# Kernel tuning notes

Hardware: AMD Instinct MI355X
Metric: run time of the kernel (lower is better)

## Reference

```python
import math
import jax, jax.numpy as jnp
import numpy as np

IMAGE_SIZE = 224


def _resize_bilinear(img, out_h, out_w):
    """PyTorch F.interpolate(mode='bilinear', align_corners=False) equivalent.
    img: [B, H, W] -> [B, out_h, out_w]. No antialiasing (matches torch default)."""
    B, H, W = img.shape

    def coords(out, size):
        r = jnp.maximum((jnp.arange(out, dtype=jnp.float32) + 0.5) * (size / out) - 0.5, 0.0)
        i0 = jnp.minimum(jnp.floor(r).astype(jnp.int32), size - 1)
        i1 = jnp.minimum(i0 + 1, size - 1)
        w = r - i0.astype(jnp.float32)
        return i0, i1, w

    r0, r1, wr = coords(out_h, H)
    c0, c1, wc = coords(out_w, W)
    rows = img[:, r0, :] * (1.0 - wr)[None, :, None] + img[:, r1, :] * wr[None, :, None]
    out = rows[:, :, c0] * (1.0 - wc)[None, None, :] + rows[:, :, c1] * wc[None, None, :]
    return out


def _normalize_minmax(x, eps=1e-8):
    mn = x.min()
    mx = x.max()
    return jnp.where(mx - mn < eps, jnp.zeros_like(x), (x - mn) / (mx - mn + eps))


def _grid_embed(vals, n):
    """Row-major scatter of vals[:, :n] into a ceil(sqrt(n))^2 grid (zero padded)."""
    B = vals.shape[0]
    gs = int(math.ceil(math.sqrt(n)))
    pad = gs * gs - n
    return jnp.pad(vals, ((0, 0), (0, pad))).reshape(B, gs, gs)


def setup_inputs() -> dict:
    key = jax.random.key(0)
    hidden_state = jax.random.normal(key, (32, 512, 4096, 1), dtype=jnp.float32)
    return {"hidden_state": hidden_state}


def reference(hidden_state):
    B, E, N, _ = hidden_state.shape
    x = hidden_state[..., 0]  # [B, E, N]

    # temporal view: mean over nodes -> [B, E] -> grid -> resize
    t_grid = _grid_embed(x.mean(axis=2), E)
    temporal = _normalize_minmax(_resize_bilinear(t_grid, IMAGE_SIZE, IMAGE_SIZE))

    # spatial view: mean over embedding dim -> [B, N] -> grid -> resize
    s_grid = _grid_embed(x.mean(axis=1), N)
    spatial = _normalize_minmax(_resize_bilinear(s_grid, IMAGE_SIZE, IMAGE_SIZE))

    # correlation view: row-normalized centered features, [B, E, E] correlation
    xc = x - x.mean(axis=2, keepdims=True)
    xn = xc / (jnp.linalg.norm(xc, axis=2, keepdims=True) + 1e-8)
    corr = jnp.einsum('bin,bjn->bij', xn, xn)  # [B, E, E]
    correlation = _normalize_minmax(_resize_bilinear(corr, IMAGE_SIZE, IMAGE_SIZE))

    # [B, 3, image_size, image_size]
    return jnp.stack([temporal, spatial, correlation], axis=1)
```

## Files before the change

kernel.cpp:

```cpp
#include <hip/hip_runtime.h>
#include <hip/hip_bf16.h>
#include <math.h>

#define IMG 224
#define PIX (IMG*IMG)
#define B_ 32
#define E_ 512
#define N_ 4096
#define SV_BLOCKS 256
#define SC_ ((float)(512.0/224.0))
#define RPB 16
#define NCHUNK 32

typedef __attribute__((ext_vector_type(8))) short bf16x8;
typedef __attribute__((ext_vector_type(4))) float f32x4;

__device__ inline unsigned short f2bf(float f){
  unsigned u = __float_as_uint(f);
  unsigned r = (u + 0x7FFFu + ((u >> 16) & 1u)) >> 16;
  return (unsigned short)r;
}

__global__ void __launch_bounds__(256) stats_y(const float* __restrict__ x,
                                               float* __restrict__ meanv,
                                               float* __restrict__ colpart,
                                               ushort* __restrict__ y){
  int b = blockIdx.x >> 5, chunk = blockIdx.x & 31;
  int e0 = chunk << 4;
  int t = threadIdx.x;
  __shared__ short sInv[512];
  __shared__ float sW[224];
  __shared__ float red[2][16];
  sInv[t] = -1; sInv[t + 256] = -1;
  __syncthreads();
  if (t < 224){
    float r = fmaxf(((float)t + 0.5f) * SC_ - 0.5f, 0.f);
    int r0 = min((int)r, E_ - 1);
    sW[t] = r - (float)r0;
    sInv[r0] = (short)t;
  }
  __syncthreads();

  float cur[16], prev[16], nxt[16], csum[16];
  #pragma unroll
  for (int j = 0; j < 16; j++){ csum[j] = 0.f; prev[j] = 0.f; }
  const float4* row0 = (const float4*)(x + ((size_t)b * E_ + e0) * N_);
  #pragma unroll
  for (int k = 0; k < 4; k++) *(float4*)(cur + 4 * k) = row0[t + 256 * k];
  float pmu = 0.f, prn = 0.f;

  for (int idx = 0; idx <= RPB; idx++){
    int e = e0 + idx;
    if (e >= E_) break;
    bool hasNext = (idx < RPB) && (e + 1 < E_);
    if (hasNext){
      const float4* nr = (const float4*)(x + ((size_t)b * E_ + e + 1) * N_);
      #pragma unroll
      for (int k = 0; k < 4; k++) *(float4*)(nxt + 4 * k) = nr[t + 256 * k];
    }
    float s = 0.f, ss = 0.f;
    #pragma unroll
    for (int j = 0; j < 16; j++){ s += cur[j]; ss += cur[j] * cur[j]; }
    #pragma unroll
    for (int o = 32; o; o >>= 1){ s += __shfl_down(s, o); ss += __shfl_down(ss, o); }
    int wv = t >> 6, ln = t & 63, p = idx & 1;
    if (ln == 0){ red[p][wv] = s; red[p][8 + wv] = ss; }
    __syncthreads();
    float S  = red[p][0] + red[p][1] + red[p][2] + red[p][3];
    float SS = red[p][8] + red[p][9] + red[p][10] + red[p][11];
    float mu = S * (1.f / N_);
    float var = fmaxf(SS - S * S * (1.f / N_), 0.f);
    float rn = 1.f / (sqrtf(var) + 1e-8f);
    if (idx < RPB){
      #pragma unroll
      for (int j = 0; j < 16; j++) csum[j] += cur[j];
      if (t == 0) meanv[b * E_ + e] = mu;
    }
    if (idx >= 1){
      int i = sInv[e - 1];
      if (i >= 0){
        float w = sW[i];
        float a0 = (1.f - w) * prn, a1 = w * rn;
        float cc = -(a0 * pmu + a1 * mu);
        ushort* yo = y + ((size_t)b * IMG + i) * N_;
        #pragma unroll
        for (int k = 0; k < 4; k++){
          union { ushort u[4]; int2 v; } pk;
          #pragma unroll
          for (int j = 0; j < 4; j++)
            pk.u[j] = f2bf(a0 * prev[4*k+j] + a1 * cur[4*k+j] + cc);
          *(int2*)(yo + 1024 * k + 4 * t) = pk.v;
        }
      }
    }
    pmu = mu; prn = rn;
    #pragma unroll
    for (int j = 0; j < 16; j++){ prev[j] = cur[j]; if (hasNext) cur[j] = nxt[j]; }
  }
  float* cp = colpart + ((size_t)(b * NCHUNK + chunk)) * N_;
  #pragma unroll
  for (int k = 0; k < 4; k++) *(float4*)(cp + 1024 * k + 4 * t) = *(float4*)(csum + 4 * k);
}

__global__ void __launch_bounds__(256) col_finalize(const float* __restrict__ colpart,
                                                    float* __restrict__ colmean){
  int b = blockIdx.x >> 4;
  int n = ((blockIdx.x & 15) << 8) + threadIdx.x;
  float s = 0.f;
  #pragma unroll
  for (int c = 0; c < NCHUNK; c++) s += colpart[((size_t)(b * NCHUNK + c)) * N_ + n];
  colmean[b * N_ + n] = s * (1.f / E_);
}

__device__ inline float grid_val(const float* v, int gs, int n, int r, int c){
  int idx = r * gs + c;
  return (idx < n) ? v[idx] : 0.f;
}
__device__ inline float bilin(const float* v, int gs, int n, int i, int j){
  float sc = (float)((double)gs / 224.0);
  float r = fmaxf(((float)i + 0.5f) * sc - 0.5f, 0.f);
  float c = fmaxf(((float)j + 0.5f) * sc - 0.5f, 0.f);
  int r0 = min((int)r, gs - 1), c0 = min((int)c, gs - 1);
  int r1 = min(r0 + 1, gs - 1), c1 = min(c0 + 1, gs - 1);
  float wr = r - (float)r0, wc = c - (float)c0;
  float v00 = grid_val(v, gs, n, r0, c0), v10 = grid_val(v, gs, n, r1, c0);
  float v01 = grid_val(v, gs, n, r0, c1), v11 = grid_val(v, gs, n, r1, c1);
  float ra = v00 * (1.f - wr) + v10 * wr;
  float rb = v01 * (1.f - wr) + v11 * wr;
  return ra * (1.f - wc) + rb * wc;
}

__global__ void __launch_bounds__(256) small_views(const float* __restrict__ meanv,
                                                   const float* __restrict__ colmean,
                                                   float* __restrict__ out,
                                                   float* __restrict__ scr){
  float tmn = INFINITY, tmx = -INFINITY, smn = INFINITY, smx = -INFINITY;
  for (int g = blockIdx.x * 256 + threadIdx.x; g < B_ * PIX; g += SV_BLOCKS * 256){
    int b = g / PIX, p = g - b * PIX;
    int i = p / IMG, j = p - i * IMG;
    float tv = bilin(meanv   + b * E_, 23, E_, i, j);
    float sv = bilin(colmean + b * N_, 64, N_, i, j);
    out[((size_t)b * 3 + 0) * PIX + p] = tv;
    out[((size_t)b * 3 + 1) * PIX + p] = sv;
    tmn = fminf(tmn, tv); tmx = fmaxf(tmx, tv);
    smn = fminf(smn, sv); smx = fmaxf(smx, sv);
  }
  #pragma unroll
  for (int o = 32; o; o >>= 1){
    tmn = fminf(tmn, __shfl_down(tmn, o)); tmx = fmaxf(tmx, __shfl_down(tmx, o));
    smn = fminf(smn, __shfl_down(smn, o)); smx = fmaxf(smx, __shfl_down(smx, o));
  }
  __shared__ float red[4][4];
  int wv = threadIdx.x >> 6, ln = threadIdx.x & 63;
  if (ln == 0){ red[wv][0] = tmn; red[wv][1] = tmx; red[wv][2] = smn; red[wv][3] = smx; }
  __syncthreads();
  if (threadIdx.x == 0){
    scr[blockIdx.x * 4 + 0] = fminf(fminf(red[0][0], red[1][0]), fminf(red[2][0], red[3][0]));
    scr[blockIdx.x * 4 + 1] = fmaxf(fmaxf(red[0][1], red[1][1]), fmaxf(red[2][1], red[3][1]));
    scr[blockIdx.x * 4 + 2] = fminf(fminf(red[0][2], red[1][2]), fminf(red[2][2], red[3][2]));
    scr[blockIdx.x * 4 + 3] = fmaxf(fmaxf(red[0][3], red[1][3]), fmaxf(red[2][3], red[3][3]));
  }
}

#define LDSTR 72
__global__ void __launch_bounds__(256) corr_gemm(const ushort* __restrict__ y,
                                                 float* __restrict__ out,
                                                 float* __restrict__ scr){
  const int TI[10] = {0,0,0,0,1,1,1,2,2,3};
  const int TJ[10] = {0,1,2,3,1,2,3,2,3,3};
  int b = blockIdx.x / 10;
  int tile = blockIdx.x - b * 10;
  int ti = TI[tile], tj = TJ[tile];
  bool diag = (ti == tj);
  const ushort* yb = y + (size_t)b * IMG * N_;
  __shared__ ushort lA[64 * LDSTR];
  __shared__ ushort lB[64 * LDSTR];
  int t = threadIdx.x;
  int wv = t >> 6, ln = t & 63;
  int wm = wv & 1, wn = wv >> 1;
  int quad = ln >> 4, l16 = ln & 15;
  f32x4 acc[2][2] = {};
  int s = t & 7, r2 = t >> 3;
  int rA0 = min(ti * 64 + r2,      223), rA1 = min(ti * 64 + r2 + 32, 223);
  int rB0 = min(tj * 64 + r2,      223), rB1 = min(tj * 64 + r2 + 32, 223);
  for (int k0 = 0; k0 < N_; k0 += 64){
    int4 a0 = *(const int4*)(yb + (size_t)rA0 * N_ + k0 + s * 8);
    int4 a1 = *(const int4*)(yb + (size_t)rA1 * N_ + k0 + s * 8);
    int4 b0v = *(const int4*)(yb + (size_t)rB0 * N_ + k0 + s * 8);
    int4 b1v = *(const int4*)(yb + (size_t)rB1 * N_ + k0 + s * 8);
    __syncthreads();
    *(int4*)(lA + r2 * LDSTR + s * 8)        = a0;
    *(int4*)(lA + (r2 + 32) * LDSTR + s * 8) = a1;
    *(int4*)(lB + r2 * LDSTR + s * 8)        = b0v;
    *(int4*)(lB + (r2 + 32) * LDSTR + s * 8) = b1v;
    __syncthreads();
    #pragma unroll
    for (int kk = 0; kk < 2; kk++){
      bf16x8 af0 = *(const bf16x8*)(lA + (wm * 32 + l16)      * LDSTR + kk * 32 + quad * 8);
      bf16x8 af1 = *(const bf16x8*)(lA + (wm * 32 + 16 + l16) * LDSTR + kk * 32 + quad * 8);
      bf16x8 bf0 = *(const bf16x8*)(lB + (wn * 32 + l16)      * LDSTR + kk * 32 + quad * 8);
      bf16x8 bf1 = *(const bf16x8*)(lB + (wn * 32 + 16 + l16) * LDSTR + kk * 32 + quad * 8);
      acc[0][0] = __builtin_amdgcn_mfma_f32_16x16x32_bf16(af0, bf0, acc[0][0], 0, 0, 0);
      acc[0][1] = __builtin_amdgcn_mfma_f32_16x16x32_bf16(af0, bf1, acc[0][1], 0, 0, 0);
      acc[1][0] = __builtin_amdgcn_mfma_f32_16x16x32_bf16(af1, bf0, acc[1][0], 0, 0, 0);
      acc[1][1] = __builtin_amdgcn_mfma_f32_16x16x32_bf16(af1, bf1, acc[1][1], 0, 0, 0);
    }
  }
  float mn = INFINITY, mx = -INFINITY;
  float* ov = out + ((size_t)b * 3 + 2) * PIX;
  #pragma unroll
  for (int im = 0; im < 2; im++)
    #pragma unroll
    for (int in = 0; in < 2; in++){
      int gi0 = ti * 64 + wm * 32 + im * 16 + quad * 4;
      int gj  = tj * 64 + wn * 32 + in * 16 + l16;
      #pragma unroll
      for (int rg = 0; rg < 4; rg++){
        int gi = gi0 + rg;
        if (gi < IMG && gj < IMG){
          float v = acc[im][in][rg];
          ov[gi * IMG + gj] = v;
          mn = fminf(mn, v); mx = fmaxf(mx, v);
        }
      }
      if (!diag && gj < IMG && gi0 < IMG){
        float4 tv;
        tv.x = acc[im][in][0]; tv.y = acc[im][in][1];
        tv.z = acc[im][in][2]; tv.w = acc[im][in][3];
        *(float4*)(ov + gj * IMG + gi0) = tv;
      }
    }
  #pragma unroll
  for (int o = 32; o; o >>= 1){
    mn = fminf(mn, __shfl_down(mn, o)); mx = fmaxf(mx, __shfl_down(mx, o));
  }
  __shared__ float red[4][2];
  if (ln == 0){ red[wv][0] = mn; red[wv][1] = mx; }
  __syncthreads();
  if (t == 0){
    scr[(b * 10 + tile) * 2 + 0] = fminf(fminf(red[0][0], red[1][0]), fminf(red[2][0], red[3][0]));
    scr[(b * 10 + tile) * 2 + 1] = fmaxf(fmaxf(red[0][1], red[1][1]), fmaxf(red[2][1], red[3][1]));
  }
}

__global__ void __launch_bounds__(256) reduce_slots(const float* __restrict__ sv_scr,
                                                    const float* __restrict__ corr_scr,
                                                    float* __restrict__ slots){
  int t = threadIdx.x;
  float tmn = sv_scr[4*t+0], tmx = sv_scr[4*t+1];
  float smn = sv_scr[4*t+2], smx = sv_scr[4*t+3];
  float cmn = INFINITY, cmx = -INFINITY;
  for (int idx = t; idx < B_ * 10; idx += 256){
    cmn = fminf(cmn, corr_scr[2*idx]);
    cmx = fmaxf(cmx, corr_scr[2*idx+1]);
  }
  #pragma unroll
  for (int o = 32; o; o >>= 1){
    tmn = fminf(tmn, __shfl_down(tmn, o)); tmx = fmaxf(tmx, __shfl_down(tmx, o));
    smn = fminf(smn, __shfl_down(smn, o)); smx = fmaxf(smx, __shfl_down(smx, o));
    cmn = fminf(cmn, __shfl_down(cmn, o)); cmx = fmaxf(cmx, __shfl_down(cmx, o));
  }
  __shared__ float red[4][6];
  int wv = t >> 6, ln = t & 63;
  if (ln == 0){
    red[wv][0]=tmn; red[wv][1]=tmx; red[wv][2]=smn;
    red[wv][3]=smx; red[wv][4]=cmn; red[wv][5]=cmx;
  }
  __syncthreads();
  if (t == 0){
    slots[0] = fminf(fminf(red[0][0],red[1][0]), fminf(red[2][0],red[3][0]));
    slots[1] = fmaxf(fmaxf(red[0][1],red[1][1]), fmaxf(red[2][1],red[3][1]));
    slots[2] = fminf(fminf(red[0][2],red[1][2]), fminf(red[2][2],red[3][2]));
    slots[3] = fmaxf(fmaxf(red[0][3],red[1][3]), fmaxf(red[2][3],red[3][3]));
    slots[4] = fminf(fminf(red[0][4],red[1][4]), fminf(red[2][4],red[3][4]));
    slots[5] = fmaxf(fmaxf(red[0][5],red[1][5]), fmaxf(red[2][5],red[3][5]));
  }
}

__global__ void __launch_bounds__(256) normalize_k(float* __restrict__ out,
                                                   const float* __restrict__ slots){
  int g = blockIdx.x * 256 + threadIdx.x;
  if (g >= B_ * 3 * PIX) return;
  int view = (g / PIX) % 3;
  float mn = slots[2 * view];
  float mx = slots[2 * view + 1];
  float d = mx - mn;
  float v = out[g];
  out[g] = (d < 1e-8f) ? 0.f : (v - mn) / (d + 1e-8f);
}

extern "C" void kernel_launch(void* const* d_in, const int* in_sizes, int n_in,
                              void* d_out, int out_size, void* d_ws, size_t ws_size,
                              hipStream_t stream){
  const float* x = (const float*)d_in[0];
  float* out = (float*)d_out;
  char* ws = (char*)d_ws;
  float* slots    = (float*)(ws + 0);
  float* meanv    = (float*)(ws + 256);
  float* colmean  = meanv + B_ * E_;
  float* colpart  = colmean + B_ * N_;
  float* sv_scr   = colpart + (size_t)B_ * NCHUNK * N_;
  float* corr_scr = sv_scr + SV_BLOCKS * 4;
  size_t y_off = ((size_t)((char*)(corr_scr + B_ * 10 * 2) - ws) + 255) & ~(size_t)255;
  ushort* y = (ushort*)(ws + y_off);

  hipLaunchKernelGGL(stats_y, dim3(B_ * NCHUNK), dim3(256), 0, stream,
                     x, meanv, colpart, y);
  hipLaunchKernelGGL(col_finalize, dim3(B_ * 16), dim3(256), 0, stream,
                     colpart, colmean);
  hipLaunchKernelGGL(small_views, dim3(SV_BLOCKS), dim3(256), 0, stream,
                     meanv, colmean, out, sv_scr);
  hipLaunchKernelGGL(corr_gemm, dim3(B_ * 10), dim3(256), 0, stream,
                     y, out, corr_scr);
  hipLaunchKernelGGL(reduce_slots, dim3(1), dim3(256), 0, stream,
                     sv_scr, corr_scr, slots);
  hipLaunchKernelGGL(normalize_k, dim3((B_ * 3 * PIX + 255) / 256), dim3(256), 0, stream,
                     out, slots);
}
```

Before: 464.1 us.

## Split correlation GEMM along K into four partial blocks plus reduce kernel

```diff
diff --git a/kernel.cpp b/kernel.cpp
--- a/kernel.cpp
+++ b/kernel.cpp
@@ -11,6 +11,9 @@
 #define SC_ ((float)(512.0/224.0))
 #define RPB 16
 #define NCHUNK 32
+#define KSPLIT 4
+#define KLEN (N_/KSPLIT)
+#define NTILE 10
 
 typedef __attribute__((ext_vector_type(8))) short bf16x8;
 typedef __attribute__((ext_vector_type(4))) float f32x4;
@@ -163,16 +166,16 @@
 }
 
 #define LDSTR 72
-__global__ void __launch_bounds__(256) corr_gemm(const ushort* __restrict__ y,
-                                                 float* __restrict__ out,
-                                                 float* __restrict__ scr){
-  const int TI[10] = {0,0,0,0,1,1,1,2,2,3};
-  const int TJ[10] = {0,1,2,3,1,2,3,2,3,3};
-  int b = blockIdx.x / 10;
-  int tile = blockIdx.x - b * 10;
-  int ti = TI[tile], tj = TJ[tile];
-  bool diag = (ti == tj);
-  const ushort* yb = y + (size_t)b * IMG * N_;
+__device__ const int TI_[NTILE] = {0,0,0,0,1,1,1,2,2,3};
+__device__ const int TJ_[NTILE] = {0,1,2,3,1,2,3,2,3,3};
+
+__global__ void __launch_bounds__(256) corr_gemm_sk(const ushort* __restrict__ y,
+                                                    float* __restrict__ partials){
+  int bt = blockIdx.x % (B_ * NTILE);
+  int ks = blockIdx.x / (B_ * NTILE);
+  int b = bt / NTILE, tile = bt - b * NTILE;
+  int ti = TI_[tile], tj = TJ_[tile];
+  const ushort* yb = y + (size_t)b * IMG * N_ + (size_t)ks * KLEN;
   __shared__ ushort lA[64 * LDSTR];
   __shared__ ushort lB[64 * LDSTR];
   int t = threadIdx.x;
@@ -183,7 +186,7 @@
   int s = t & 7, r2 = t >> 3;
   int rA0 = min(ti * 64 + r2,      223), rA1 = min(ti * 64 + r2 + 32, 223);
   int rB0 = min(tj * 64 + r2,      223), rB1 = min(tj * 64 + r2 + 32, 223);
-  for (int k0 = 0; k0 < N_; k0 += 64){
+  for (int k0 = 0; k0 < KLEN; k0 += 64){
     int4 a0 = *(const int4*)(yb + (size_t)rA0 * N_ + k0 + s * 8);
     int4 a1 = *(const int4*)(yb + (size_t)rA1 * N_ + k0 + s * 8);
     int4 b0v = *(const int4*)(yb + (size_t)rB0 * N_ + k0 + s * 8);
@@ -206,6 +209,37 @@
       acc[1][1] = __builtin_amdgcn_mfma_f32_16x16x32_bf16(af1, bf1, acc[1][1], 0, 0, 0);
     }
   }
+  float* pp = partials + ((size_t)ks * (B_ * NTILE) + bt) * 4096 + t * 16;
+  #pragma unroll
+  for (int im = 0; im < 2; im++)
+    #pragma unroll
+    for (int in = 0; in < 2; in++)
+      *(f32x4*)(pp + 4 * (im * 2 + in)) = acc[im][in];
+}
+
+__global__ void __launch_bounds__(256) corr_reduce(const float* __restrict__ partials,
+                                                   float* __restrict__ out,
+                                                   float* __restrict__ scr){
+  int bt = blockIdx.x;
+  int b = bt / NTILE, tile = bt - b * NTILE;
+  int ti = TI_[tile], tj = TJ_[tile];
+  bool diag = (ti == tj);
+  int t = threadIdx.x;
+  int wv = t >> 6, ln = t & 63;
+  int wm = wv & 1, wn = wv >> 1;
+  int quad = ln >> 4, l16 = ln & 15;
+  f32x4 acc[2][2];
+  #pragma unroll
+  for (int im = 0; im < 2; im++)
+    #pragma unroll
+    for (int in = 0; in < 2; in++){
+      f32x4 a = {0.f, 0.f, 0.f, 0.f};
+      #pragma unroll
+      for (int ks = 0; ks < KSPLIT; ks++)
+        a += *(const f32x4*)(partials + ((size_t)ks * (B_ * NTILE) + bt) * 4096
+                             + t * 16 + 4 * (im * 2 + in));
+      acc[im][in] = a;
+    }
   float mn = INFINITY, mx = -INFINITY;
   float* ov = out + ((size_t)b * 3 + 2) * PIX;
   #pragma unroll
@@ -238,8 +272,8 @@
   if (ln == 0){ red[wv][0] = mn; red[wv][1] = mx; }
   __syncthreads();
   if (t == 0){
-    scr[(b * 10 + tile) * 2 + 0] = fminf(fminf(red[0][0], red[1][0]), fminf(red[2][0], red[3][0]));
-    scr[(b * 10 + tile) * 2 + 1] = fmaxf(fmaxf(red[0][1], red[1][1]), fmaxf(red[2][1], red[3][1]));
+    scr[bt * 2 + 0] = fminf(fminf(red[0][0], red[1][0]), fminf(red[2][0], red[3][0]));
+    scr[bt * 2 + 1] = fmaxf(fmaxf(red[0][1], red[1][1]), fmaxf(red[2][1], red[3][1]));
   }
 }
 
@@ -250,7 +284,7 @@
   float tmn = sv_scr[4*t+0], tmx = sv_scr[4*t+1];
   float smn = sv_scr[4*t+2], smx = sv_scr[4*t+3];
   float cmn = INFINITY, cmx = -INFINITY;
-  for (int idx = t; idx < B_ * 10; idx += 256){
+  for (int idx = t; idx < B_ * NTILE; idx += 256){
     cmn = fminf(cmn, corr_scr[2*idx]);
     cmx = fmaxf(cmx, corr_scr[2*idx+1]);
   }
@@ -301,17 +335,21 @@
   float* colpart  = colmean + B_ * N_;
   float* sv_scr   = colpart + (size_t)B_ * NCHUNK * N_;
   float* corr_scr = sv_scr + SV_BLOCKS * 4;
-  size_t y_off = ((size_t)((char*)(corr_scr + B_ * 10 * 2) - ws) + 255) & ~(size_t)255;
+  size_t y_off = ((size_t)((char*)(corr_scr + B_ * NTILE * 2) - ws) + 255) & ~(size_t)255;
   ushort* y = (ushort*)(ws + y_off);
+  size_t p_off = (y_off + (size_t)B_ * IMG * N_ * 2 + 255) & ~(size_t)255;
+  float* partials = (float*)(ws + p_off);
 
   hipLaunchKernelGGL(stats_y, dim3(B_ * NCHUNK), dim3(256), 0, stream,
                      x, meanv, colpart, y);
+  hipLaunchKernelGGL(corr_gemm_sk, dim3(KSPLIT * B_ * NTILE), dim3(256), 0, stream,
+                     y, partials);
+  hipLaunchKernelGGL(corr_reduce, dim3(B_ * NTILE), dim3(256), 0, stream,
+                     partials, out, corr_scr);
   hipLaunchKernelGGL(col_finalize, dim3(B_ * 16), dim3(256), 0, stream,
                      colpart, colmean);
   hipLaunchKernelGGL(small_views, dim3(SV_BLOCKS), dim3(256), 0, stream,
                      meanv, colmean, out, sv_scr);
-  hipLaunchKernelGGL(corr_gemm, dim3(B_ * 10), dim3(256), 0, stream,
-                     y, out, corr_scr);
   hipLaunchKernelGGL(reduce_slots, dim3(1), dim3(256), 0, stream,
                      sv_scr, corr_scr, slots);
   hipLaunchKernelGGL(normalize_k, dim3((B_ * 3 * PIX + 255) / 256), dim3(256), 0, stream,
```

Measured after the change: 450.8 us. 2.9% less time.
